# Kernel tuning notes

Measured on AMD Instinct MI355X. Metric: run time of the kernel, lower is better.

Reference implementation:

```python
import jax, jax.numpy as jnp
import numpy as np

Z = 20000      # batch (e.g., graph nodes)
U = 128        # segment multiplicity ('u' mode)
S = 8          # segments per operand (same for all 4 operands here)
P = 64         # number of paths


def setup_inputs() -> dict:
    key = jax.random.key(0)
    k0, k1, k2, kc, ki = jax.random.split(key, 5)
    x0 = jax.random.normal(k0, (Z, S * U), dtype=jnp.float32)
    x1 = jax.random.normal(k1, (Z, S * U), dtype=jnp.float32)
    x2 = jax.random.normal(k2, (Z, S * U), dtype=jnp.float32)
    path_coefficients = jax.random.normal(kc, (P,), dtype=jnp.float32)
    # each path picks one segment index per operand (op0, op1, op2, output)
    path_indices = jax.random.randint(ki, (P, 4), 0, S, dtype=jnp.int32)
    return {"x0": x0, "x1": x1, "x2": x2,
            "path_coefficients": path_coefficients,
            "path_indices": path_indices}


def reference(x0, x1, x2, path_coefficients, path_indices):
    # Segmented tensor product, channelwise mode 'u,u,u->u':
    # out[z, i3, u] += sum_p c[p] * x0[z, i0[p], u] * x1[z, i1[p], u] * x2[z, i2[p], u]
    x0s = x0.reshape(Z, S, U)
    x1s = x1.reshape(Z, S, U)
    x2s = x2.reshape(Z, S, U)
    i0, i1, i2, i3 = (path_indices[:, 0], path_indices[:, 1],
                      path_indices[:, 2], path_indices[:, 3])
    # gather segments per path: [Z, P, U]
    prod = (x0s[:, i0, :] * x1s[:, i1, :] * x2s[:, i2, :]
            * path_coefficients[None, :, None])
    # scatter-add paths into output segments: [S, Z, U]
    out = jax.ops.segment_sum(jnp.swapaxes(prod, 0, 1), i3, num_segments=S)
    return jnp.swapaxes(out, 0, 1).reshape(Z, S * U)
```

## Files before the change

### kernel.cpp

```cpp
#include <hip/hip_runtime.h>

constexpr int Zn = 20000;
constexpr int Un = 128;
constexpr int Sn = 8;
constexpr int Pn = 64;
constexpr int ROW = Sn * Un;
constexpr int ZPB = 4;
constexpr int THREADS = 128;

__global__ void prep_kernel(const int* __restrict__ pi,
                            const float* __restrict__ pc,
                            int4* __restrict__ table,
                            int* __restrict__ segstart) {
    if (threadIdx.x != 0 || blockIdx.x != 0) return;
    int cnt[Sn];
    for (int s = 0; s < Sn; ++s) cnt[s] = 0;
    for (int p = 0; p < Pn; ++p) cnt[pi[4 * p + 3]]++;
    int off[Sn + 1];
    off[0] = 0;
    for (int s = 0; s < Sn; ++s) off[s + 1] = off[s] + cnt[s];
    for (int s = 0; s <= Sn; ++s) segstart[s] = off[s];
    int cur[Sn];
    for (int s = 0; s < Sn; ++s) cur[s] = off[s];
    for (int p = 0; p < Pn; ++p) {
        int s3 = pi[4 * p + 3];
        int slot = cur[s3]++;
        table[slot] = make_int4(pi[4 * p + 0] * Un,
                                ROW + pi[4 * p + 1] * Un,
                                2 * ROW + pi[4 * p + 2] * Un,
                                __float_as_int(pc[p]));
    }
}

__global__ __launch_bounds__(THREADS) void tp_kernel(
        const float* __restrict__ x0,
        const float* __restrict__ x1,
        const float* __restrict__ x2,
        const int4* __restrict__ table,
        const int* __restrict__ segstart,
        float* __restrict__ out) {
    __shared__ __align__(16) float lds[ZPB * 3 * ROW];
    const int tid = threadIdx.x;
    const int zblk = blockIdx.x * ZPB;

    {
        const float* srcs[3] = { x0, x1, x2 };
#pragma unroll
        for (int t = 0; t < 3; ++t) {
            const float4* src = (const float4*)(srcs[t] + (size_t)zblk * ROW);
            float4* dst = (float4*)lds;
#pragma unroll
            for (int i = 0; i < (ZPB * (ROW / 4)) / THREADS; ++i) {
                int idx = i * THREADS + tid;
                int z = idx >> 8;
                int r = idx & 255;
                dst[(z * 3 + t) * (ROW / 4) + r] = src[z * (ROW / 4) + r];
            }
        }
    }
    __syncthreads();

    int ss[Sn + 1];
#pragma unroll
    for (int i = 0; i <= Sn; ++i) ss[i] = segstart[i];

    const int lane = tid & 63;
    const int wave = tid >> 6;
    const int zloc = wave * 2 + (lane >> 5);
    const int u4   = (lane & 31);
    const float* zb = lds + zloc * (3 * ROW);
    float* orow = out + (size_t)(zblk + zloc) * ROW;

#pragma unroll
    for (int seg = 0; seg < Sn; ++seg) {
        float4 acc = make_float4(0.f, 0.f, 0.f, 0.f);
        for (int k = ss[seg]; k < ss[seg + 1]; ++k) {
            int4 e = table[k];
            const float4 a = *(const float4*)(zb + e.x + u4 * 4);
            const float4 b = *(const float4*)(zb + e.y + u4 * 4);
            const float4 c = *(const float4*)(zb + e.z + u4 * 4);
            const float w = __int_as_float(e.w);
            acc.x += a.x * b.x * c.x * w;
            acc.y += a.y * b.y * c.y * w;
            acc.z += a.z * b.z * c.z * w;
            acc.w += a.w * b.w * c.w * w;
        }
        *(float4*)(orow + seg * Un + u4 * 4) = acc;
    }
}

extern "C" void kernel_launch(void* const* d_in, const int* in_sizes, int n_in,
                              void* d_out, int out_size, void* d_ws, size_t ws_size,
                              hipStream_t stream) {
    const float* x0 = (const float*)d_in[0];
    const float* x1 = (const float*)d_in[1];
    const float* x2 = (const float*)d_in[2];
    const float* pc = (const float*)d_in[3];
    const int*   pi = (const int*)d_in[4];
    float* out = (float*)d_out;

    int4* table   = (int4*)d_ws;
    int*  segstart = (int*)((char*)d_ws + Pn * sizeof(int4));

    prep_kernel<<<1, 1, 0, stream>>>(pi, pc, table, segstart);
    tp_kernel<<<Zn / ZPB, THREADS, 0, stream>>>(x0, x1, x2, table, segstart, out);
}
```

Baseline: 284.8 us.

## Parallelize prep with wave ballots and split output segments across waves

Result: faster. 276.8 us (-2.8%).

```diff
diff --git a/kernel.cpp b/kernel.cpp
--- a/kernel.cpp
+++ b/kernel.cpp
@@ -5,57 +5,58 @@
 constexpr int Sn = 8;
 constexpr int Pn = 64;
 constexpr int ROW = Sn * Un;
-constexpr int ZPB = 4;
+constexpr int ZPB = 2;
 constexpr int THREADS = 128;
 
-__global__ void prep_kernel(const int* __restrict__ pi,
-                            const float* __restrict__ pc,
-                            int4* __restrict__ table,
-                            int* __restrict__ segstart) {
-    if (threadIdx.x != 0 || blockIdx.x != 0) return;
-    int cnt[Sn];
-    for (int s = 0; s < Sn; ++s) cnt[s] = 0;
-    for (int p = 0; p < Pn; ++p) cnt[pi[4 * p + 3]]++;
-    int off[Sn + 1];
-    off[0] = 0;
-    for (int s = 0; s < Sn; ++s) off[s + 1] = off[s] + cnt[s];
-    for (int s = 0; s <= Sn; ++s) segstart[s] = off[s];
-    int cur[Sn];
-    for (int s = 0; s < Sn; ++s) cur[s] = off[s];
-    for (int p = 0; p < Pn; ++p) {
-        int s3 = pi[4 * p + 3];
-        int slot = cur[s3]++;
-        table[slot] = make_int4(pi[4 * p + 0] * Un,
-                                ROW + pi[4 * p + 1] * Un,
-                                2 * ROW + pi[4 * p + 2] * Un,
-                                __float_as_int(pc[p]));
+__global__ __launch_bounds__(64) void prep_kernel(const int* __restrict__ pi,
+                                                  const float* __restrict__ pc,
+                                                  int4* __restrict__ table,
+                                                  int* __restrict__ segstart) {
+    const int p = threadIdx.x & 63;
+    const int i0 = pi[4 * p + 0];
+    const int i1 = pi[4 * p + 1];
+    const int i2 = pi[4 * p + 2];
+    const int i3 = pi[4 * p + 3];
+    const float w = pc[p];
+    const unsigned long long below = (1ull << p) - 1ull;
+
+    int base = 0, slot = 0;
+#pragma unroll
+    for (int s = 0; s < Sn; ++s) {
+        unsigned long long m = __ballot(i3 == s);
+        if (i3 == s) slot = base + __popcll(m & below);
+        if (p == 0) segstart[s] = base;
+        base += __popcll(m);
     }
+    if (p == 0) segstart[Sn] = base;
+
+    table[slot] = make_int4(i0 * Un,
+                            ZPB * ROW + i1 * Un,
+                            2 * ZPB * ROW + i2 * Un,
+                            __float_as_int(w));
 }
 
-__global__ __launch_bounds__(THREADS) void tp_kernel(
+__global__ __launch_bounds__(THREADS, 3) void tp_kernel(
         const float* __restrict__ x0,
         const float* __restrict__ x1,
         const float* __restrict__ x2,
         const int4* __restrict__ table,
         const int* __restrict__ segstart,
         float* __restrict__ out) {
-    __shared__ __align__(16) float lds[ZPB * 3 * ROW];
+    __shared__ __align__(16) float lds[3 * ZPB * ROW];
     const int tid = threadIdx.x;
     const int zblk = blockIdx.x * ZPB;
 
-    {
-        const float* srcs[3] = { x0, x1, x2 };
 #pragma unroll
-        for (int t = 0; t < 3; ++t) {
-            const float4* src = (const float4*)(srcs[t] + (size_t)zblk * ROW);
-            float4* dst = (float4*)lds;
+    for (int t = 0; t < 3; ++t) {
+        const float4* src = (const float4*)(t == 0 ? x0 : (t == 1 ? x1 : x2));
+        float4* dst = (float4*)lds + t * (ZPB * ROW / 4);
 #pragma unroll
-            for (int i = 0; i < (ZPB * (ROW / 4)) / THREADS; ++i) {
-                int idx = i * THREADS + tid;
-                int z = idx >> 8;
-                int r = idx & 255;
-                dst[(z * 3 + t) * (ROW / 4) + r] = src[z * (ROW / 4) + r];
-            }
+        for (int i = 0; i < (ZPB * ROW / 4) / THREADS; ++i) {
+            int local = i * THREADS + tid;
+            int z = local >> 8;
+            int r = local & 255;
+            dst[local] = src[(size_t)(zblk + z) * (ROW / 4) + r];
         }
     }
     __syncthreads();
@@ -66,15 +67,15 @@
 
     const int lane = tid & 63;
     const int wave = tid >> 6;
-    const int zloc = wave * 2 + (lane >> 5);
-    const int u4   = (lane & 31);
-    const float* zb = lds + zloc * (3 * ROW);
+    const int zloc = lane >> 5;
+    const int u4   = lane & 31;
+    const float* zb = lds + zloc * ROW;
     float* orow = out + (size_t)(zblk + zloc) * ROW;
 
 #pragma unroll
-    for (int seg = 0; seg < Sn; ++seg) {
+    for (int s = wave * (Sn / 2); s < (wave + 1) * (Sn / 2); ++s) {
         float4 acc = make_float4(0.f, 0.f, 0.f, 0.f);
-        for (int k = ss[seg]; k < ss[seg + 1]; ++k) {
+        for (int k = ss[s]; k < ss[s + 1]; ++k) {
             int4 e = table[k];
             const float4 a = *(const float4*)(zb + e.x + u4 * 4);
             const float4 b = *(const float4*)(zb + e.y + u4 * 4);
@@ -85,7 +86,7 @@
             acc.z += a.z * b.z * c.z * w;
             acc.w += a.w * b.w * c.w * w;
         }
-        *(float4*)(orow + seg * Un + u4 * 4) = acc;
+        *(float4*)(orow + s * Un + u4 * 4) = acc;
     }
 }
 
@@ -99,9 +100,9 @@
     const int*   pi = (const int*)d_in[4];
     float* out = (float*)d_out;
 
-    int4* table   = (int4*)d_ws;
+    int4* table    = (int4*)d_ws;
     int*  segstart = (int*)((char*)d_ws + Pn * sizeof(int4));
 
-    prep_kernel<<<1, 1, 0, stream>>>(pi, pc, table, segstart);
+    prep_kernel<<<1, 64, 0, stream>>>(pi, pc, table, segstart);
     tp_kernel<<<Zn / ZPB, THREADS, 0, stream>>>(x0, x1, x2, table, segstart, out);
 }
```
